# Kernel tuning notes

Hardware: AMD Instinct MI355X
Metric: run time of the kernel (lower is better)

The kernel has to match this reference:

```python
import jax, jax.numpy as jnp
import numpy as np

B, T = 16, 64
A = 6              # num_actions
E = 12288          # embed_size
DET = 4096         # deter_size
HID = 1024         # hidden_size
S, D = 32, 32      # stoch_size, discrete
UM = 0.01          # uniform_mix
CLIP = 1.0         # action_clip
EPS = 1e-3         # LayerNorm eps


def _ln(x, g, b):
    m = jnp.mean(x, -1, keepdims=True)
    v = jnp.var(x, -1, keepdims=True)
    return (x - m) * jax.lax.rsqrt(v + EPS) * g + b


def setup_inputs() -> dict:
    key = jax.random.key(0)
    ks = jax.random.split(key, 24)
    w = lambda k, i, o: (jax.random.normal(k, (i, o), jnp.float32) / np.sqrt(i))
    gum = lambda k, shp: -jnp.log(-jnp.log(jax.random.uniform(k, shp, jnp.float32, 1e-6, 1.0 - 1e-6)))
    is_firsts = (jax.random.uniform(ks[2], (B, T)) < 0.05).astype(jnp.float32)
    is_firsts = is_firsts.at[:, 0].set(1.0)
    return {
        'embed': jax.random.normal(ks[0], (B, T, E), jnp.float32),
        'prev_actions': jax.random.normal(ks[1], (B, T, A), jnp.float32),
        'is_firsts': is_firsts,
        'gumbel_prior': gum(ks[3], (B, T, S, D)),
        'gumbel_post': gum(ks[4], (B, T, S, D)),
        'w_init': jnp.zeros((DET,), jnp.float32),
        'W_img1': w(ks[5], S * D + A, HID), 'g_img1': jnp.ones((HID,)), 'b_img1': jnp.zeros((HID,)),
        'W_gru': w(ks[6], HID + DET, 3 * DET), 'g_gru': jnp.ones((3 * DET,)), 'b_gru': jnp.zeros((3 * DET,)),
        'W_img2a': w(ks[7], DET, HID), 'g_img2': jnp.ones((HID,)), 'b_img2': jnp.zeros((HID,)),
        'W_img2b': w(ks[8], HID, S * D), 'bb_img2': jnp.zeros((S * D,)),
        'W_obs': w(ks[9], E + DET, HID), 'g_obs': jnp.ones((HID,)), 'b_obs': jnp.zeros((HID,)),
        'W_obsb': w(ks[10], HID, S * D), 'bb_obs': jnp.zeros((S * D,)),
    }


def reference(embed, prev_actions, is_firsts, gumbel_prior, gumbel_post,
              w_init, W_img1, g_img1, b_img1, W_gru, g_gru, b_gru,
              W_img2a, g_img2, b_img2, W_img2b, bb_img2,
              W_obs, g_obs, b_obs, W_obsb, bb_obs):
    sg = jax.lax.stop_gradient

    def clip_act(a):
        return a * sg(CLIP / jnp.maximum(jnp.abs(a), CLIP))

    def prior_logits(deter):  # mlp_img2
        h = jax.nn.silu(_ln(deter @ W_img2a, g_img2, b_img2))
        return (h @ W_img2b + bb_img2).reshape(deter.shape[:-1] + (S, D))

    def mix_probs(logits):  # OneHotDist uniform mix
        p = jax.nn.softmax(logits, -1)
        return (1.0 - UM) * p + UM / D

    def st_sample(logits, g):  # straight-through gumbel-max sample
        p = mix_probs(logits)
        oh = jax.nn.one_hot(jnp.argmax(jnp.log(p) + g, -1), D, dtype=logits.dtype)
        return oh + p - sg(p)

    def st_mode(logits):
        p = mix_probs(logits)
        oh = jax.nn.one_hot(jnp.argmax(p, -1), D, dtype=logits.dtype)
        return oh + p - sg(p)

    # learned initial state (initial(): deter=tanh(w), stoch=mode, logits=0)
    init_deter = jnp.broadcast_to(jnp.tanh(w_init)[None], (B, DET))
    init_stoch = st_mode(prior_logits(init_deter))

    # observe() with prev_state=None zeroes the first action and starts from initial state
    prev_actions = prev_actions.at[:, 0].set(0.0)

    def step(carry, xs):
        stoch, deter, logits_post = carry
        a, e, f, gp, gq = xs
        a = clip_act(a)                                  # clip in forward()
        f1 = f[:, None]
        f3 = f[:, None, None]
        a = a * (1.0 - f1)
        stoch = stoch * (1.0 - f3) + init_stoch * f3
        deter = deter * (1.0 - f1) + init_deter * f1
        logits_post = logits_post * (1.0 - f3)           # initial logits are zeros
        a = clip_act(a)                                  # clipped again in forward_img()
        # mlp_img1
        x = jax.nn.silu(_ln(jnp.concatenate([stoch.reshape(B, S * D), a], -1) @ W_img1, g_img1, b_img1))
        # DreamerV2 GRU cell: single LN-linear -> reset/cand/update
        parts = _ln(jnp.concatenate([x, deter], -1) @ W_gru, g_gru, b_gru)
        reset, cand, update = jnp.split(parts, 3, -1)
        reset = jax.nn.sigmoid(reset)
        cand = jnp.tanh(reset * cand)
        update = jax.nn.sigmoid(update - 1.0)
        deter_new = update * cand + (1.0 - update) * deter
        # prior head
        lp = prior_logits(deter_new)
        stoch_prior = st_sample(lp, gp)
        # posterior head (mlp_obs1)
        h2 = jax.nn.silu(_ln(jnp.concatenate([e, deter_new], -1) @ W_obs, g_obs, b_obs))
        lq = (h2 @ W_obsb + bb_obs).reshape(B, S, D)
        stoch_post = st_sample(lq, gq)
        return (stoch_post, deter_new, lq), (stoch_post, deter_new, lq, stoch_prior, lp)

    carry0 = (init_stoch, init_deter, jnp.zeros((B, S, D), embed.dtype))
    xs = (jnp.swapaxes(prev_actions, 0, 1), jnp.swapaxes(embed, 0, 1), jnp.swapaxes(is_firsts, 0, 1),
          jnp.swapaxes(gumbel_prior, 0, 1), jnp.swapaxes(gumbel_post, 0, 1))
    _, outs = jax.lax.scan(step, carry0, xs)
    post_stoch, post_deter, post_logits, prior_stoch, prior_lg = [jnp.swapaxes(o, 0, 1) for o in outs]
    # pack posts and priors (prior deter == post deter) into one array [B,T,8192]
    return jnp.concatenate([post_stoch.reshape(B, T, S * D), post_deter,
                            post_logits.reshape(B, T, S * D),
                            prior_stoch.reshape(B, T, S * D),
                            prior_lg.reshape(B, T, S * D)], -1)
```

## Files before the change

### kernel.cpp

```cpp
#include <hip/hip_runtime.h>
#include <cmath>


#define B 16
#define T_STEPS 64
#define A_DIM 6
#define E_DIM 12288
#define DET 4096
#define HID 1024
#define SD 1024
#define OUT_C 8192
#define OUT_RSTRIDE (T_STEPS * OUT_C)

typedef float f2v __attribute__((ext_vector_type(2)));

__device__ __forceinline__ float block_sum(float v, float* red, int nw) {
#pragma unroll
  for (int m = 32; m >= 1; m >>= 1) v += __shfl_xor(v, m, 64);
  int wid = threadIdx.x >> 6;
  if ((threadIdx.x & 63) == 0) red[wid] = v;
  __syncthreads();
  if (wid == 0) {
    float s = ((int)threadIdx.x < nw) ? red[threadIdx.x] : 0.0f;
#pragma unroll
    for (int m = 8; m >= 1; m >>= 1) s += __shfl_xor(s, m, 16);
    if (threadIdx.x == 0) red[0] = s;
  }
  __syncthreads();
  float out = red[0];
  __syncthreads();
  return out;
}

__global__ __launch_bounds__(1024) void k_tanh(const float* __restrict__ w, float* __restrict__ o) {
  int i = blockIdx.x * 1024 + threadIdx.x;
  if (i < DET) o[i] = tanhf(w[i]);
}

__global__ __launch_bounds__(256) void k_prep(
    const float* __restrict__ isf, const float* __restrict__ pa, int t,
    const float* __restrict__ stoch_prev,
    const float* __restrict__ deter_prev, long deter_prev_stride,
    const float* __restrict__ init_stoch, const float* __restrict__ init_deter_row,
    float* __restrict__ stoch_in, float* __restrict__ deter_in, float* __restrict__ a_eff) {
  int r = blockIdx.x;
  float f = isf[r * T_STEPS + t];
  float omf = 1.0f - f;
  for (int c = threadIdx.x; c < SD; c += 256)
    stoch_in[r * SD + c] = stoch_prev[r * SD + c] * omf + init_stoch[r * SD + c] * f;
  for (int c = threadIdx.x; c < DET; c += 256)
    deter_in[r * DET + c] = deter_prev[(long)r * deter_prev_stride + c] * omf + init_deter_row[c] * f;
  if ((int)threadIdx.x < A_DIM) {
    float a = pa[(r * T_STEPS + t) * A_DIM + threadIdx.x];
    a = a * (1.0f / fmaxf(fabsf(a), 1.0f));
    a_eff[r * 8 + threadIdx.x] = a * omf;
  }
}

struct GemmArgs {
  const float* A0; long sA0; int cA0;
  const float* A1; long sA1;
  const float* W; int N; int Ktot; int KS; int nsplit;
  float* P;
};

template <bool NT>
__global__ __launch_bounds__(256) void k_gemm(GemmArgs g) {
  if ((int)blockIdx.y >= g.nsplit) return;
  const int tid = threadIdx.x;
  const int c0 = blockIdx.x * 512 + tid * 2;
  const int k0 = (int)blockIdx.y * g.KS;
  __shared__ float in_s[16][64];
  float acc[16][2];
#pragma unroll
  for (int r = 0; r < 16; r++) { acc[r][0] = 0.f; acc[r][1] = 0.f; }
  for (int kb = 0; kb < g.KS; kb += 64) {
    const int kbase = k0 + kb;
#pragma unroll
    for (int j = 0; j < 4; j++) {
      int ii = tid + j * 256;
      int r = ii >> 6, kk = ii & 63;
      int k = kbase + kk;
      float v = 0.f;
      if (k < g.cA0) v = g.A0[(long)r * g.sA0 + k];
      else if (k < g.Ktot) v = g.A1[(long)r * g.sA1 + (k - g.cA0)];
      in_s[r][kk] = v;
    }
    __syncthreads();
    if (kbase + 64 <= g.Ktot) {
      const float* wp = g.W + (size_t)kbase * g.N + c0;
#pragma unroll 4
      for (int kk = 0; kk < 64; kk++) {
        f2v w = NT ? __builtin_nontemporal_load((const f2v*)wp) : *(const f2v*)wp;
        wp += g.N;
#pragma unroll
        for (int r = 0; r < 16; r++) {
          acc[r][0] += in_s[r][kk] * w[0]; acc[r][1] += in_s[r][kk] * w[1];
        }
      }
    } else {
#pragma unroll 4
      for (int kk = 0; kk < 64; kk++) {
        int krow = kbase + kk; if (krow >= g.Ktot) krow = g.Ktot - 1;
        const f2v w = *(const f2v*)(g.W + (size_t)krow * g.N + c0);
#pragma unroll
        for (int r = 0; r < 16; r++) {
          acc[r][0] += in_s[r][kk] * w[0]; acc[r][1] += in_s[r][kk] * w[1];
        }
      }
    }
    __syncthreads();
  }
#pragma unroll
  for (int r = 0; r < 16; r++)
    *(f2v*)(g.P + ((size_t)blockIdx.y * 16 + r) * g.N + c0) = f2v{acc[r][0], acc[r][1]};
}

__global__ __launch_bounds__(1024) void k_fin(
    const float* __restrict__ P, int nP,
    const float* __restrict__ add, long ads,
    const float* __restrict__ gv, const float* __restrict__ bv,
    float* __restrict__ o) {
  int r = blockIdx.x, c = threadIdx.x;
  __shared__ float red[18];
  float v = add ? add[(size_t)r * ads + c] : 0.0f;
  for (int ks = 0; ks < nP; ks++) v += P[((size_t)ks * 16 + r) * HID + c];
  float m = block_sum(v, red, 16) * (1.0f / (float)HID);
  float d = v - m;
  float var = block_sum(d * d, red, 16) * (1.0f / (float)HID);
  float rs = 1.0f / sqrtf(var + 1e-3f);
  float y = d * rs * gv[c] + bv[c];
  float s = 1.0f / (1.0f + expf(-y));
  o[r * HID + c] = y * s;
}

__global__ __launch_bounds__(1024) void k_samp_init(
    const float* __restrict__ P, int nP, const float* __restrict__ bb,
    float* __restrict__ st) {
  int r = blockIdx.x, c = threadIdx.x;
  float acc = bb[c];
  for (int ks = 0; ks < nP; ks++) acc += P[((size_t)ks * 16 + r) * SD + c];
  int d = c & 31;
  float mx = acc;
#pragma unroll
  for (int m = 16; m >= 1; m >>= 1) mx = fmaxf(mx, __shfl_xor(mx, m, 32));
  float e = expf(acc - mx);
  float se = e;
#pragma unroll
  for (int m = 16; m >= 1; m >>= 1) se += __shfl_xor(se, m, 32);
  float p = 0.99f * (e / se) + 3.125e-4f;
  float by = p; int bi = d;
#pragma unroll
  for (int m = 16; m >= 1; m >>= 1) {
    float oy = __shfl_xor(by, m, 32);
    int oi = __shfl_xor(bi, m, 32);
    if (oy > by || (oy == by && oi < bi)) { by = oy; bi = oi; }
  }
  float oh = (d == bi) ? 1.0f : 0.0f;
  st[r * SD + c] = (oh + p) - p;
}

__global__ __launch_bounds__(256) void k_mm(const float* __restrict__ A, long lda,
                                            const float* __restrict__ Bw, int K,
                                            float* __restrict__ out, long ldo,
                                            const float* __restrict__ bias) {
  __shared__ float As[32][68];
  __shared__ float Bs[32][68];
  const int tid = threadIdx.x;
  const int tx = tid & 15, ty = tid >> 4;
  const int row0 = blockIdx.y * 64, col0 = blockIdx.x * 64;
  const int ar = tid >> 2, ak = (tid & 3) * 8;
  const int bk = tid >> 4, bc = (tid & 15) * 4;
  float acc[4][4] = {};
  const float* ap = A + (size_t)(row0 + ar) * lda + ak;
  const float* bp = Bw + (size_t)bk * HID + col0 + bc;
  for (int k0 = 0; k0 < K; k0 += 32) {
    float4 a0 = *(const float4*)(ap + k0);
    float4 a1 = *(const float4*)(ap + k0 + 4);
    float4 b0 = *(const float4*)(bp + (size_t)k0 * HID);
    float4 b1 = *(const float4*)(bp + (size_t)(k0 + 16) * HID);
    __syncthreads();
    As[ak + 0][ar] = a0.x; As[ak + 1][ar] = a0.y; As[ak + 2][ar] = a0.z; As[ak + 3][ar] = a0.w;
    As[ak + 4][ar] = a1.x; As[ak + 5][ar] = a1.y; As[ak + 6][ar] = a1.z; As[ak + 7][ar] = a1.w;
    *(float4*)&Bs[bk][bc] = b0;
    *(float4*)&Bs[bk + 16][bc] = b1;
    __syncthreads();
#pragma unroll
    for (int kk = 0; kk < 32; kk++) {
      float4 av = *(const float4*)&As[kk][ty * 4];
      float4 bv = *(const float4*)&Bs[kk][tx * 4];
      acc[0][0] += av.x * bv.x; acc[0][1] += av.x * bv.y; acc[0][2] += av.x * bv.z; acc[0][3] += av.x * bv.w;
      acc[1][0] += av.y * bv.x; acc[1][1] += av.y * bv.y; acc[1][2] += av.y * bv.z; acc[1][3] += av.y * bv.w;
      acc[2][0] += av.z * bv.x; acc[2][1] += av.z * bv.y; acc[2][2] += av.z * bv.z; acc[2][3] += av.z * bv.w;
      acc[3][0] += av.w * bv.x; acc[3][1] += av.w * bv.y; acc[3][2] += av.w * bv.z; acc[3][3] += av.w * bv.w;
    }
  }
#pragma unroll
  for (int i = 0; i < 4; i++) {
    float4 o;
    int col = col0 + tx * 4;
    o.x = acc[i][0] + (bias ? bias[col + 0] : 0.f);
    o.y = acc[i][1] + (bias ? bias[col + 1] : 0.f);
    o.z = acc[i][2] + (bias ? bias[col + 2] : 0.f);
    o.w = acc[i][3] + (bias ? bias[col + 3] : 0.f);
    *(float4*)(out + (size_t)(row0 + ty * 4 + i) * ldo + col) = o;
  }
}

__global__ __launch_bounds__(256) void k_ln_rows(float* __restrict__ h,
                                                 const float* __restrict__ gv,
                                                 const float* __restrict__ bv) {
  int row = blockIdx.x, c0 = threadIdx.x * 4;
  __shared__ float red[18];
  float4 v = *(const float4*)(h + (size_t)row * HID + c0);
  float lsum = (v.x + v.y) + (v.z + v.w);
  float m = block_sum(lsum, red, 4) * (1.0f / (float)HID);
  float dx = v.x - m, dy = v.y - m, dz = v.z - m, dw = v.w - m;
  float lv = (dx * dx + dy * dy) + (dz * dz + dw * dw);
  float var = block_sum(lv, red, 4) * (1.0f / (float)HID);
  float rs = 1.0f / sqrtf(var + 1e-3f);
  float4 o;
  float y0 = dx * rs * gv[c0] + bv[c0];         o.x = y0 / (1.0f + expf(-y0));
  float y1 = dy * rs * gv[c0 + 1] + bv[c0 + 1]; o.y = y1 / (1.0f + expf(-y1));
  float y2 = dz * rs * gv[c0 + 2] + bv[c0 + 2]; o.z = y2 / (1.0f + expf(-y2));
  float y3 = dw * rs * gv[c0 + 3] + bv[c0 + 3]; o.w = y3 / (1.0f + expf(-y3));
  *(float4*)(h + (size_t)row * HID + c0) = o;
}

__global__ __launch_bounds__(1024) void k_samp_prior(float* __restrict__ out,
                                                     const float* __restrict__ gum) {
  int m = blockIdx.x, c = threadIdx.x;
  float lp = out[(size_t)m * OUT_C + 7168 + c];
  int d = c & 31;
  float mx = lp;
#pragma unroll
  for (int mm = 16; mm >= 1; mm >>= 1) mx = fmaxf(mx, __shfl_xor(mx, mm, 32));
  float e = expf(lp - mx);
  float se = e;
#pragma unroll
  for (int mm = 16; mm >= 1; mm >>= 1) se += __shfl_xor(se, mm, 32);
  float p = 0.99f * (e / se) + 3.125e-4f;
  float y = logf(p) + gum[(size_t)m * SD + c];
  float by = y; int bi = d;
#pragma unroll
  for (int mm = 16; mm >= 1; mm >>= 1) {
    float oy = __shfl_xor(by, mm, 32);
    int oi = __shfl_xor(bi, mm, 32);
    if (oy > by || (oy == by && oi < bi)) { by = oy; bi = oi; }
  }
  float oh = (d == bi) ? 1.0f : 0.0f;
  out[(size_t)m * OUT_C + 6144 + c] = (oh + p) - p;
}

__global__ __launch_bounds__(256) void k_red(const float* __restrict__ P, int nP,
                                             float* __restrict__ S,
                                             float* __restrict__ red_s, float* __restrict__ red_q) {
  int chunk = blockIdx.x, r = blockIdx.y;
  int c = chunk * 1024 + threadIdx.x * 4;
  float4 s = {0, 0, 0, 0};
  for (int ks = 0; ks < nP; ks++) {
    float4 v = *(const float4*)(P + ((size_t)ks * 16 + r) * (3 * DET) + c);
    s.x += v.x; s.y += v.y; s.z += v.z; s.w += v.w;
  }
  *(float4*)(S + (size_t)r * (3 * DET) + c) = s;
  float sx = (s.x + s.y) + (s.z + s.w);
  float sq = (s.x * s.x + s.y * s.y) + (s.z * s.z + s.w * s.w);
  __shared__ float rbuf[8];
#pragma unroll
  for (int m = 32; m >= 1; m >>= 1) { sx += __shfl_xor(sx, m, 64); sq += __shfl_xor(sq, m, 64); }
  int wid = threadIdx.x >> 6;
  if ((threadIdx.x & 63) == 0) { rbuf[wid] = sx; rbuf[4 + wid] = sq; }
  __syncthreads();
  if (threadIdx.x == 0) {
    red_s[r * 12 + chunk] = (rbuf[0] + rbuf[1]) + (rbuf[2] + rbuf[3]);
    red_q[r * 12 + chunk] = (rbuf[4] + rbuf[5]) + (rbuf[6] + rbuf[7]);
  }
}

__global__ __launch_bounds__(1024) void k_gru_gate(
    const float* __restrict__ S, const float* __restrict__ red_s, const float* __restrict__ red_q,
    const float* __restrict__ g, const float* __restrict__ b,
    float* __restrict__ deter_in, float* __restrict__ deter_new,
    float* __restrict__ out_deter, const float* __restrict__ isf, int t,
    const float* __restrict__ init_deter) {
  int r = blockIdx.x;
  __shared__ float mv[2];
  if (threadIdx.x == 0) {
    float s = 0.f, q = 0.f;
    for (int k2 = 0; k2 < 12; k2++) { s += red_s[r * 12 + k2]; q += red_q[r * 12 + k2]; }
    float m = s * (1.0f / (float)(3 * DET));
    float var = q * (1.0f / (float)(3 * DET)) - m * m;
    mv[0] = m; mv[1] = 1.0f / sqrtf(var + 1e-3f);
  }
  __syncthreads();
  float m = mv[0], rs = mv[1];
  float ft = (t + 1 < T_STEPS) ? isf[r * T_STEPS + t + 1] : 0.0f;
  for (int j = threadIdx.x; j < DET; j += 1024) {
    float lr = (S[(size_t)r * (3 * DET) + j] - m) * rs * g[j] + b[j];
    float lc = (S[(size_t)r * (3 * DET) + j + DET] - m) * rs * g[j + DET] + b[j + DET];
    float lu = (S[(size_t)r * (3 * DET) + j + 2 * DET] - m) * rs * g[j + 2 * DET] + b[j + 2 * DET];
    float rr = 1.0f / (1.0f + expf(-lr));
    float cd = tanhf(rr * lc);
    float uu = 1.0f / (1.0f + expf(-(lu - 1.0f)));
    float dn = uu * cd + (1.0f - uu) * deter_in[r * DET + j];
    deter_new[r * DET + j] = dn;
    out_deter[(size_t)r * OUT_RSTRIDE + j] = dn;
    deter_in[r * DET + j] = dn * (1.0f - ft) + init_deter[j] * ft;
  }
}

__global__ __launch_bounds__(1024) void k_samp(
    const float* __restrict__ P, int nP, const float* __restrict__ bb,
    const float* __restrict__ gum, long gs,
    float* __restrict__ st, long ss, float* __restrict__ lg, long ls,
    const float* __restrict__ isf, const float* __restrict__ pa, int t,
    float* __restrict__ stoch_in, float* __restrict__ a_eff,
    const float* __restrict__ init_stoch) {
  int r = blockIdx.x, c = threadIdx.x;
  float acc = bb[c];
  for (int ks = 0; ks < nP; ks++) acc += P[((size_t)ks * 16 + r) * SD + c];
  int d = c & 31;
  float mx = acc;
#pragma unroll
  for (int m = 16; m >= 1; m >>= 1) mx = fmaxf(mx, __shfl_xor(mx, m, 32));
  float e = expf(acc - mx);
  float se = e;
#pragma unroll
  for (int m = 16; m >= 1; m >>= 1) se += __shfl_xor(se, m, 32);
  float p = 0.99f * (e / se) + 3.125e-4f;
  float y = logf(p) + gum[(long)r * gs + c];
  float by = y; int bi = d;
#pragma unroll
  for (int m = 16; m >= 1; m >>= 1) {
    float oy = __shfl_xor(by, m, 32);
    int oi = __shfl_xor(bi, m, 32);
    if (oy > by || (oy == by && oi < bi)) { by = oy; bi = oi; }
  }
  float oh = (d == bi) ? 1.0f : 0.0f;
  float outv = (oh + p) - p;
  st[(long)r * ss + c] = outv;
  lg[(long)r * ls + c] = acc;
  float fn = (t + 1 < T_STEPS) ? isf[r * T_STEPS + t + 1] : 0.0f;
  stoch_in[r * SD + c] = outv * (1.0f - fn) + init_stoch[r * SD + c] * fn;
  if (c < A_DIM) {
    float a = (t + 1 < T_STEPS) ? pa[(r * T_STEPS + t + 1) * A_DIM + c] : 0.0f;
    a = a * (1.0f / fmaxf(fabsf(a), 1.0f));
    a_eff[r * 8 + c] = a * (1.0f - fn);
  }
}

static inline GemmArgs mkargs(const float* A0, long sA0, int cA0,
                              const float* A1, long sA1,
                              const float* W, int N, int Ktot, int KS, int nsplit, float* P) {
  GemmArgs g; g.A0 = A0; g.sA0 = sA0; g.cA0 = cA0; g.A1 = A1; g.sA1 = sA1;
  g.W = W; g.N = N; g.Ktot = Ktot; g.KS = KS; g.nsplit = nsplit; g.P = P;
  return g;
}

extern "C" void kernel_launch(void* const* d_in, const int* in_sizes, int n_in,
                              void* d_out, int out_size, void* d_ws, size_t ws_size,
                              hipStream_t stream) {
  const float* embed  = (const float*)d_in[0];
  const float* pa     = (const float*)d_in[1];
  const float* isf    = (const float*)d_in[2];
  const float* gprior = (const float*)d_in[3];
  const float* gpost  = (const float*)d_in[4];
  const float* w_init = (const float*)d_in[5];
  const float* W1  = (const float*)d_in[6];
  const float* g1  = (const float*)d_in[7];
  const float* b1  = (const float*)d_in[8];
  const float* Wg  = (const float*)d_in[9];
  const float* gg  = (const float*)d_in[10];
  const float* bg  = (const float*)d_in[11];
  const float* W2a = (const float*)d_in[12];
  const float* g2  = (const float*)d_in[13];
  const float* b2  = (const float*)d_in[14];
  const float* W2b = (const float*)d_in[15];
  const float* bb2 = (const float*)d_in[16];
  const float* Wo  = (const float*)d_in[17];
  const float* go  = (const float*)d_in[18];
  const float* bo  = (const float*)d_in[19];
  const float* Wob = (const float*)d_in[20];
  const float* bbo = (const float*)d_in[21];
  float* out = (float*)d_out;
  float* ws  = (float*)d_ws;

  float* Pg    = ws;
  float* h_all = Pg;
  float* Sg    = Pg + 3932160;
  float* red_s = Sg + 196608;
  float* red_q = red_s + 192;
  float* Pimg1 = red_s + 512;
  float* Pb    = Pimg1 + 278528;
  float* Ps1   = Pb + 524288;
  float* st_   = Ps1 + 262144;
  float* init_stoch = st_;
  float* init_deter = st_ + 16384;
  float* stoch_in   = st_ + 20480;
  float* deter_in   = st_ + 36864;
  float* deter_new  = st_ + 102400;
  float* a_eff      = st_ + 167936;
  float* x          = st_ + 168064;
  float* h2         = st_ + 184448;

  k_mm<<<dim3(16, 16), 256, 0, stream>>>(embed, E_DIM, Wo, E_DIM, out + 5120, OUT_C, nullptr);

  k_tanh<<<4, 1024, 0, stream>>>(w_init, init_deter);
  k_gemm<true><<<dim3(2, 32), 256, 0, stream>>>(
      mkargs(init_deter, 0, DET, nullptr, 0, W2a, HID, DET, 128, 32, Pb));
  k_fin<<<16, 1024, 0, stream>>>(Pb, 32, nullptr, 0, g2, b2, x);
  k_gemm<true><<<dim3(2, 16), 256, 0, stream>>>(
      mkargs(x, HID, HID, nullptr, 0, W2b, SD, HID, 64, 16, Ps1));
  k_samp_init<<<16, 1024, 0, stream>>>(Ps1, 16, bb2, init_stoch);

  k_prep<<<16, 256, 0, stream>>>(isf, pa, 0, init_stoch, init_deter, 0,
                                 init_stoch, init_deter, stoch_in, deter_in, a_eff);

  for (int t = 0; t < T_STEPS; t++) {
    k_gemm<true><<<dim3(2, 17), 256, 0, stream>>>(
        mkargs(stoch_in, SD, SD, a_eff, 8, W1, HID, SD + A_DIM, 64, 17, Pimg1));
    k_fin<<<16, 1024, 0, stream>>>(Pimg1, 17, nullptr, 0, g1, b1, x);
    k_gemm<false><<<dim3(24, 20), 256, 0, stream>>>(
        mkargs(x, HID, HID, deter_in, DET, Wg, 3 * DET, HID + DET, 256, 20, Pg));
    k_red<<<dim3(12, 16), 256, 0, stream>>>(Pg, 20, Sg, red_s, red_q);
    k_gru_gate<<<16, 1024, 0, stream>>>(Sg, red_s, red_q, gg, bg, deter_in, deter_new,
                                        out + (size_t)t * OUT_C + 1024, isf, t, init_deter);
    k_gemm<true><<<dim3(2, 32), 256, 0, stream>>>(
        mkargs(deter_new, DET, DET, nullptr, 0, Wo + (size_t)E_DIM * HID, HID, DET, 128, 32, Pb));
    k_fin<<<16, 1024, 0, stream>>>(Pb, 32, out + (size_t)t * OUT_C + 5120, OUT_RSTRIDE,
                                   go, bo, h2);
    k_gemm<true><<<dim3(2, 16), 256, 0, stream>>>(
        mkargs(h2, HID, HID, nullptr, 0, Wob, SD, HID, 64, 16, Ps1));
    k_samp<<<16, 1024, 0, stream>>>(
        Ps1, 16, bbo, gpost + (size_t)t * SD, (long)T_STEPS * SD,
        out + (size_t)t * OUT_C + 0, OUT_RSTRIDE,
        out + (size_t)t * OUT_C + 5120, OUT_RSTRIDE,
        isf, pa, t, stoch_in, a_eff, init_stoch);
  }

  k_mm<<<dim3(16, 16), 256, 0, stream>>>(out + 1024, OUT_C, W2a, DET, h_all, HID, nullptr);
  k_ln_rows<<<1024, 256, 0, stream>>>(h_all, g2, b2);
  k_mm<<<dim3(16, 16), 256, 0, stream>>>(h_all, HID, W2b, HID, out + 7168, OUT_C, bb2);
  k_samp_prior<<<1024, 1024, 0, stream>>>(out, gprior);
}
```

Measured before the change: 11.30 ms.

## Fuse per-step GEMMs with their reductions via last-block atomic counters

Inside the time loop, the split-K GEMM launches and their follow-up reduce/LayerNorm/sampling kernels are merged into single kernels. In each one, the last block to finish (found with an atomic counter) sums the partials and applies the epilogue. The GRU gate is computed inside the obs-GEMM blocks, with deter_in ping-ponged between two buffers. This cuts per-step kernel launches from 9 to 5 and removes several launch gaps. The costs are that gate math is repeated across both column tiles, the final reduction runs on a single block, and correctness now depends on threadfence and atomic ordering.

```diff
diff --git a/kernel.cpp b/kernel.cpp
--- a/kernel.cpp
+++ b/kernel.cpp
@@ -13,6 +13,7 @@
 #define OUT_RSTRIDE (T_STEPS * OUT_C)
 
 typedef float f2v __attribute__((ext_vector_type(2)));
+typedef float f4v __attribute__((ext_vector_type(4)));
 
 __device__ __forceinline__ float block_sum(float v, float* red, int nw) {
 #pragma unroll
@@ -66,7 +67,6 @@
 
 template <bool NT>
 __global__ __launch_bounds__(256) void k_gemm(GemmArgs g) {
-  if ((int)blockIdx.y >= g.nsplit) return;
   const int tid = threadIdx.x;
   const int c0 = blockIdx.x * 512 + tid * 2;
   const int k0 = (int)blockIdx.y * g.KS;
@@ -118,12 +118,11 @@
 
 __global__ __launch_bounds__(1024) void k_fin(
     const float* __restrict__ P, int nP,
-    const float* __restrict__ add, long ads,
     const float* __restrict__ gv, const float* __restrict__ bv,
     float* __restrict__ o) {
   int r = blockIdx.x, c = threadIdx.x;
   __shared__ float red[18];
-  float v = add ? add[(size_t)r * ads + c] : 0.0f;
+  float v = 0.0f;
   for (int ks = 0; ks < nP; ks++) v += P[((size_t)ks * 16 + r) * HID + c];
   float m = block_sum(v, red, 16) * (1.0f / (float)HID);
   float d = v - m;
@@ -277,75 +276,267 @@
   }
 }
 
-__global__ __launch_bounds__(1024) void k_gru_gate(
-    const float* __restrict__ S, const float* __restrict__ red_s, const float* __restrict__ red_q,
-    const float* __restrict__ g, const float* __restrict__ b,
-    float* __restrict__ deter_in, float* __restrict__ deter_new,
-    float* __restrict__ out_deter, const float* __restrict__ isf, int t,
-    const float* __restrict__ init_deter) {
-  int r = blockIdx.x;
-  __shared__ float mv[2];
-  if (threadIdx.x == 0) {
+
+__global__ __launch_bounds__(256) void k_img1f(
+    const float* __restrict__ stoch_in, const float* __restrict__ a_eff,
+    const float* __restrict__ W, const float* __restrict__ gv, const float* __restrict__ bv,
+    float* __restrict__ P, float* __restrict__ xout, unsigned int* __restrict__ cnt) {
+  const int tid = threadIdx.x;
+  const int c0 = blockIdx.x * 512 + tid * 2;
+  const int kbase = (int)blockIdx.y * 64;
+  __shared__ float in_s[16][64];
+  __shared__ float red[18];
+  __shared__ unsigned int lastv;
+  float acc[16][2];
+#pragma unroll
+  for (int r = 0; r < 16; r++) { acc[r][0] = 0.f; acc[r][1] = 0.f; }
+#pragma unroll
+  for (int j = 0; j < 4; j++) {
+    int ii = tid + j * 256;
+    int r = ii >> 6, kk = ii & 63;
+    int k = kbase + kk;
+    float v = 0.f;
+    if (k < SD) v = stoch_in[r * SD + k];
+    else if (k < SD + A_DIM) v = a_eff[r * 8 + (k - SD)];
+    in_s[r][kk] = v;
+  }
+  __syncthreads();
+  if (kbase + 64 <= SD + A_DIM) {
+    const float* wp = W + (size_t)kbase * HID + c0;
+#pragma unroll 4
+    for (int kk = 0; kk < 64; kk++) {
+      f2v w = __builtin_nontemporal_load((const f2v*)wp);
+      wp += HID;
+#pragma unroll
+      for (int r = 0; r < 16; r++) {
+        acc[r][0] += in_s[r][kk] * w[0]; acc[r][1] += in_s[r][kk] * w[1];
+      }
+    }
+  } else {
+#pragma unroll 4
+    for (int kk = 0; kk < 64; kk++) {
+      int krow = kbase + kk; if (krow >= SD + A_DIM) krow = SD + A_DIM - 1;
+      const f2v w = *(const f2v*)(W + (size_t)krow * HID + c0);
+#pragma unroll
+      for (int r = 0; r < 16; r++) {
+        acc[r][0] += in_s[r][kk] * w[0]; acc[r][1] += in_s[r][kk] * w[1];
+      }
+    }
+  }
+#pragma unroll
+  for (int r = 0; r < 16; r++)
+    *(f2v*)(P + ((size_t)blockIdx.y * 16 + r) * HID + c0) = f2v{acc[r][0], acc[r][1]};
+  __threadfence();
+  __syncthreads();
+  if (tid == 0) lastv = atomicAdd(cnt, 1u);
+  __syncthreads();
+  if (lastv == 34u - 1u) {
+    if (tid == 0) atomicExch(cnt, 0u);
+    __threadfence();
+    const int c = tid * 4;
+    for (int r = 0; r < 16; r++) {
+      f4v v = {0, 0, 0, 0};
+      for (int ks = 0; ks < 17; ks++) {
+        f4v pv = *(const f4v*)(P + ((size_t)ks * 16 + r) * HID + c);
+        v[0] += pv[0]; v[1] += pv[1]; v[2] += pv[2]; v[3] += pv[3];
+      }
+      float lsum = (v[0] + v[1]) + (v[2] + v[3]);
+      float m = block_sum(lsum, red, 4) * (1.0f / (float)HID);
+      float d0 = v[0] - m, d1 = v[1] - m, d2 = v[2] - m, d3 = v[3] - m;
+      float lv = (d0 * d0 + d1 * d1) + (d2 * d2 + d3 * d3);
+      float var = block_sum(lv, red, 4) * (1.0f / (float)HID);
+      float rs = 1.0f / sqrtf(var + 1e-3f);
+      float dd[4] = {d0, d1, d2, d3};
+      f4v o;
+#pragma unroll
+      for (int j = 0; j < 4; j++) {
+        float y = dd[j] * rs * gv[c + j] + bv[c + j];
+        o[j] = y / (1.0f + expf(-y));
+      }
+      *(f4v*)(xout + (size_t)r * HID + c) = o;
+    }
+  }
+}
+
+__global__ __launch_bounds__(256) void k_obsf(
+    const float* __restrict__ Sg, const float* __restrict__ red_s, const float* __restrict__ red_q,
+    const float* __restrict__ gg, const float* __restrict__ bg,
+    const float* __restrict__ din_cur, float* __restrict__ din_next,
+    const float* __restrict__ init_deter, const float* __restrict__ isf, int t,
+    const float* __restrict__ W, const float* __restrict__ gv, const float* __restrict__ bv,
+    float* __restrict__ out, float* __restrict__ h2,
+    float* __restrict__ P, unsigned int* __restrict__ cnt) {
+  const int tid = threadIdx.x;
+  const int tile = blockIdx.x;
+  const int split = blockIdx.y;
+  const int c0 = tile * 512 + tid * 2;
+  const int j0 = split * 128;
+  __shared__ float dn_s[16][128];
+  __shared__ float mvf[16][3];
+  __shared__ float red[18];
+  __shared__ unsigned int lastv;
+  if (tid < 16) {
+    int r = tid;
     float s = 0.f, q = 0.f;
     for (int k2 = 0; k2 < 12; k2++) { s += red_s[r * 12 + k2]; q += red_q[r * 12 + k2]; }
     float m = s * (1.0f / (float)(3 * DET));
     float var = q * (1.0f / (float)(3 * DET)) - m * m;
-    mv[0] = m; mv[1] = 1.0f / sqrtf(var + 1e-3f);
-  }
-  __syncthreads();
-  float m = mv[0], rs = mv[1];
-  float ft = (t + 1 < T_STEPS) ? isf[r * T_STEPS + t + 1] : 0.0f;
-  for (int j = threadIdx.x; j < DET; j += 1024) {
-    float lr = (S[(size_t)r * (3 * DET) + j] - m) * rs * g[j] + b[j];
-    float lc = (S[(size_t)r * (3 * DET) + j + DET] - m) * rs * g[j + DET] + b[j + DET];
-    float lu = (S[(size_t)r * (3 * DET) + j + 2 * DET] - m) * rs * g[j + 2 * DET] + b[j + 2 * DET];
+    mvf[r][0] = m; mvf[r][1] = 1.0f / sqrtf(var + 1e-3f);
+    mvf[r][2] = (t + 1 < T_STEPS) ? isf[r * T_STEPS + t + 1] : 0.0f;
+  }
+  __syncthreads();
+  for (int e = tid; e < 16 * 128; e += 256) {
+    int r = e >> 7, jj = e & 127;
+    int j = j0 + jj;
+    float m = mvf[r][0], rs = mvf[r][1];
+    const float* Sr = Sg + (size_t)r * (3 * DET);
+    float lr = (Sr[j] - m) * rs * gg[j] + bg[j];
+    float lc = (Sr[j + DET] - m) * rs * gg[j + DET] + bg[j + DET];
+    float lu = (Sr[j + 2 * DET] - m) * rs * gg[j + 2 * DET] + bg[j + 2 * DET];
     float rr = 1.0f / (1.0f + expf(-lr));
     float cd = tanhf(rr * lc);
     float uu = 1.0f / (1.0f + expf(-(lu - 1.0f)));
-    float dn = uu * cd + (1.0f - uu) * deter_in[r * DET + j];
-    deter_new[r * DET + j] = dn;
-    out_deter[(size_t)r * OUT_RSTRIDE + j] = dn;
-    deter_in[r * DET + j] = dn * (1.0f - ft) + init_deter[j] * ft;
-  }
-}
-
-__global__ __launch_bounds__(1024) void k_samp(
-    const float* __restrict__ P, int nP, const float* __restrict__ bb,
-    const float* __restrict__ gum, long gs,
-    float* __restrict__ st, long ss, float* __restrict__ lg, long ls,
-    const float* __restrict__ isf, const float* __restrict__ pa, int t,
+    float dn = uu * cd + (1.0f - uu) * din_cur[r * DET + j];
+    dn_s[r][jj] = dn;
+    if (tile == 0) {
+      out[(size_t)(r * T_STEPS + t) * OUT_C + 1024 + j] = dn;
+      float ft = mvf[r][2];
+      din_next[r * DET + j] = dn * (1.0f - ft) + init_deter[j] * ft;
+    }
+  }
+  __syncthreads();
+  float acc[16][2];
+#pragma unroll
+  for (int r = 0; r < 16; r++) { acc[r][0] = 0.f; acc[r][1] = 0.f; }
+  for (int kb = 0; kb < 128; kb += 64) {
+    const float* wp = W + (size_t)(j0 + kb) * HID + c0;
+#pragma unroll 4
+    for (int kk = 0; kk < 64; kk++) {
+      f2v w = __builtin_nontemporal_load((const f2v*)wp);
+      wp += HID;
+#pragma unroll
+      for (int r = 0; r < 16; r++) {
+        float iv = dn_s[r][kb + kk];
+        acc[r][0] += iv * w[0]; acc[r][1] += iv * w[1];
+      }
+    }
+  }
+#pragma unroll
+  for (int r = 0; r < 16; r++)
+    *(f2v*)(P + ((size_t)split * 16 + r) * HID + c0) = f2v{acc[r][0], acc[r][1]};
+  __threadfence();
+  __syncthreads();
+  if (tid == 0) lastv = atomicAdd(cnt, 1u);
+  __syncthreads();
+  if (lastv == 64u - 1u) {
+    if (tid == 0) atomicExch(cnt, 0u);
+    __threadfence();
+    const int c = tid * 4;
+    for (int r = 0; r < 16; r++) {
+      f4v v = *(const f4v*)(out + (size_t)(r * T_STEPS + t) * OUT_C + 5120 + c);
+      for (int ks = 0; ks < 32; ks++) {
+        f4v pv = *(const f4v*)(P + ((size_t)ks * 16 + r) * HID + c);
+        v[0] += pv[0]; v[1] += pv[1]; v[2] += pv[2]; v[3] += pv[3];
+      }
+      float lsum = (v[0] + v[1]) + (v[2] + v[3]);
+      float m = block_sum(lsum, red, 4) * (1.0f / (float)HID);
+      float d0 = v[0] - m, d1 = v[1] - m, d2 = v[2] - m, d3 = v[3] - m;
+      float lv = (d0 * d0 + d1 * d1) + (d2 * d2 + d3 * d3);
+      float var = block_sum(lv, red, 4) * (1.0f / (float)HID);
+      float rs = 1.0f / sqrtf(var + 1e-3f);
+      float dd[4] = {d0, d1, d2, d3};
+      f4v o;
+#pragma unroll
+      for (int j = 0; j < 4; j++) {
+        float y = dd[j] * rs * gv[c + j] + bv[c + j];
+        o[j] = y / (1.0f + expf(-y));
+      }
+      *(f4v*)(h2 + (size_t)r * HID + c) = o;
+    }
+  }
+}
+
+__global__ __launch_bounds__(256) void k_postf(
+    const float* __restrict__ h2, const float* __restrict__ W,
+    const float* __restrict__ bb, const float* __restrict__ gum, long gs,
+    float* __restrict__ out, int t,
+    const float* __restrict__ isf, const float* __restrict__ pa,
     float* __restrict__ stoch_in, float* __restrict__ a_eff,
-    const float* __restrict__ init_stoch) {
-  int r = blockIdx.x, c = threadIdx.x;
-  float acc = bb[c];
-  for (int ks = 0; ks < nP; ks++) acc += P[((size_t)ks * 16 + r) * SD + c];
-  int d = c & 31;
-  float mx = acc;
-#pragma unroll
-  for (int m = 16; m >= 1; m >>= 1) mx = fmaxf(mx, __shfl_xor(mx, m, 32));
-  float e = expf(acc - mx);
-  float se = e;
-#pragma unroll
-  for (int m = 16; m >= 1; m >>= 1) se += __shfl_xor(se, m, 32);
-  float p = 0.99f * (e / se) + 3.125e-4f;
-  float y = logf(p) + gum[(long)r * gs + c];
-  float by = y; int bi = d;
-#pragma unroll
-  for (int m = 16; m >= 1; m >>= 1) {
-    float oy = __shfl_xor(by, m, 32);
-    int oi = __shfl_xor(bi, m, 32);
-    if (oy > by || (oy == by && oi < bi)) { by = oy; bi = oi; }
-  }
-  float oh = (d == bi) ? 1.0f : 0.0f;
-  float outv = (oh + p) - p;
-  st[(long)r * ss + c] = outv;
-  lg[(long)r * ls + c] = acc;
-  float fn = (t + 1 < T_STEPS) ? isf[r * T_STEPS + t + 1] : 0.0f;
-  stoch_in[r * SD + c] = outv * (1.0f - fn) + init_stoch[r * SD + c] * fn;
-  if (c < A_DIM) {
-    float a = (t + 1 < T_STEPS) ? pa[(r * T_STEPS + t + 1) * A_DIM + c] : 0.0f;
-    a = a * (1.0f / fmaxf(fabsf(a), 1.0f));
-    a_eff[r * 8 + c] = a * (1.0f - fn);
+    const float* __restrict__ init_stoch,
+    float* __restrict__ P, unsigned int* __restrict__ cnt) {
+  const int tid = threadIdx.x;
+  const int c0 = blockIdx.x * 512 + tid * 2;
+  const int kbase = (int)blockIdx.y * 64;
+  __shared__ float in_s[16][64];
+  __shared__ unsigned int lastv;
+  float acc[16][2];
+#pragma unroll
+  for (int r = 0; r < 16; r++) { acc[r][0] = 0.f; acc[r][1] = 0.f; }
+#pragma unroll
+  for (int j = 0; j < 4; j++) {
+    int ii = tid + j * 256;
+    int r = ii >> 6, kk = ii & 63;
+    in_s[r][kk] = h2[r * HID + kbase + kk];
+  }
+  __syncthreads();
+  {
+    const float* wp = W + (size_t)kbase * SD + c0;
+#pragma unroll 4
+    for (int kk = 0; kk < 64; kk++) {
+      f2v w = __builtin_nontemporal_load((const f2v*)wp);
+      wp += SD;
+#pragma unroll
+      for (int r = 0; r < 16; r++) {
+        acc[r][0] += in_s[r][kk] * w[0]; acc[r][1] += in_s[r][kk] * w[1];
+      }
+    }
+  }
+#pragma unroll
+  for (int r = 0; r < 16; r++)
+    *(f2v*)(P + ((size_t)blockIdx.y * 16 + r) * SD + c0) = f2v{acc[r][0], acc[r][1]};
+  __threadfence();
+  __syncthreads();
+  if (tid == 0) lastv = atomicAdd(cnt, 1u);
+  __syncthreads();
+  if (lastv == 32u - 1u) {
+    if (tid == 0) atomicExch(cnt, 0u);
+    __threadfence();
+    const int d = tid & 31;
+    for (int it = 0; it < 64; it++) {
+      int gi = it * 8 + (tid >> 5);
+      int r = gi >> 5, grp = gi & 31;
+      int c = grp * 32 + d;
+      float a = bb[c];
+      for (int ks = 0; ks < 16; ks++) a += P[((size_t)ks * 16 + r) * SD + c];
+      float mx = a;
+#pragma unroll
+      for (int m = 16; m >= 1; m >>= 1) mx = fmaxf(mx, __shfl_xor(mx, m, 32));
+      float e = expf(a - mx);
+      float se = e;
+#pragma unroll
+      for (int m = 16; m >= 1; m >>= 1) se += __shfl_xor(se, m, 32);
+      float p = 0.99f * (e / se) + 3.125e-4f;
+      float y = logf(p) + gum[(long)r * gs + c];
+      float by = y; int bi = d;
+#pragma unroll
+      for (int m = 16; m >= 1; m >>= 1) {
+        float oy = __shfl_xor(by, m, 32);
+        int oi = __shfl_xor(bi, m, 32);
+        if (oy > by || (oy == by && oi < bi)) { by = oy; bi = oi; }
+      }
+      float oh = (d == bi) ? 1.0f : 0.0f;
+      float outv = (oh + p) - p;
+      float* ob = out + (size_t)(r * T_STEPS + t) * OUT_C;
+      ob[c] = outv;
+      ob[5120 + c] = a;
+      float fn = (t + 1 < T_STEPS) ? isf[r * T_STEPS + t + 1] : 0.0f;
+      stoch_in[r * SD + c] = outv * (1.0f - fn) + init_stoch[r * SD + c] * fn;
+      if (c < A_DIM) {
+        float av = (t + 1 < T_STEPS) ? pa[(r * T_STEPS + t + 1) * A_DIM + c] : 0.0f;
+        av = av * (1.0f / fmaxf(fabsf(av), 1.0f));
+        a_eff[r * 8 + c] = av * (1.0f - fn);
+      }
+    }
   }
 }
 
@@ -390,6 +581,7 @@
   float* Sg    = Pg + 3932160;
   float* red_s = Sg + 196608;
   float* red_q = red_s + 192;
+  unsigned int* cnts = (unsigned int*)(red_s + 384);
   float* Pimg1 = red_s + 512;
   float* Pb    = Pimg1 + 278528;
   float* Ps1   = Pb + 524288;
@@ -397,45 +589,42 @@
   float* init_stoch = st_;
   float* init_deter = st_ + 16384;
   float* stoch_in   = st_ + 20480;
-  float* deter_in   = st_ + 36864;
-  float* deter_new  = st_ + 102400;
+  float* din0       = st_ + 36864;
+  float* din1       = st_ + 102400;
   float* a_eff      = st_ + 167936;
   float* x          = st_ + 168064;
   float* h2         = st_ + 184448;
 
+  hipMemsetAsync(cnts, 0, 64, stream);
+
   k_mm<<<dim3(16, 16), 256, 0, stream>>>(embed, E_DIM, Wo, E_DIM, out + 5120, OUT_C, nullptr);
 
   k_tanh<<<4, 1024, 0, stream>>>(w_init, init_deter);
   k_gemm<true><<<dim3(2, 32), 256, 0, stream>>>(
       mkargs(init_deter, 0, DET, nullptr, 0, W2a, HID, DET, 128, 32, Pb));
-  k_fin<<<16, 1024, 0, stream>>>(Pb, 32, nullptr, 0, g2, b2, x);
+  k_fin<<<16, 1024, 0, stream>>>(Pb, 32, g2, b2, x);
   k_gemm<true><<<dim3(2, 16), 256, 0, stream>>>(
       mkargs(x, HID, HID, nullptr, 0, W2b, SD, HID, 64, 16, Ps1));
   k_samp_init<<<16, 1024, 0, stream>>>(Ps1, 16, bb2, init_stoch);
 
   k_prep<<<16, 256, 0, stream>>>(isf, pa, 0, init_stoch, init_deter, 0,
-                                 init_stoch, init_deter, stoch_in, deter_in, a_eff);
-
+                                 init_stoch, init_deter, stoch_in, din0, a_eff);
+
+  const float* Wo2 = Wo + (size_t)E_DIM * HID;
   for (int t = 0; t < T_STEPS; t++) {
-    k_gemm<true><<<dim3(2, 17), 256, 0, stream>>>(
-        mkargs(stoch_in, SD, SD, a_eff, 8, W1, HID, SD + A_DIM, 64, 17, Pimg1));
-    k_fin<<<16, 1024, 0, stream>>>(Pimg1, 17, nullptr, 0, g1, b1, x);
+    float* din_cur  = (t & 1) ? din1 : din0;
+    float* din_next = (t & 1) ? din0 : din1;
+    k_img1f<<<dim3(2, 17), 256, 0, stream>>>(stoch_in, a_eff, W1, g1, b1, Pimg1, x, cnts + 0);
     k_gemm<false><<<dim3(24, 20), 256, 0, stream>>>(
-        mkargs(x, HID, HID, deter_in, DET, Wg, 3 * DET, HID + DET, 256, 20, Pg));
+        mkargs(x, HID, HID, din_cur, DET, Wg, 3 * DET, HID + DET, 256, 20, Pg));
     k_red<<<dim3(12, 16), 256, 0, stream>>>(Pg, 20, Sg, red_s, red_q);
-    k_gru_gate<<<16, 1024, 0, stream>>>(Sg, red_s, red_q, gg, bg, deter_in, deter_new,
-                                        out + (size_t)t * OUT_C + 1024, isf, t, init_deter);
-    k_gemm<true><<<dim3(2, 32), 256, 0, stream>>>(
-        mkargs(deter_new, DET, DET, nullptr, 0, Wo + (size_t)E_DIM * HID, HID, DET, 128, 32, Pb));
-    k_fin<<<16, 1024, 0, stream>>>(Pb, 32, out + (size_t)t * OUT_C + 5120, OUT_RSTRIDE,
-                                   go, bo, h2);
-    k_gemm<true><<<dim3(2, 16), 256, 0, stream>>>(
-        mkargs(h2, HID, HID, nullptr, 0, Wob, SD, HID, 64, 16, Ps1));
-    k_samp<<<16, 1024, 0, stream>>>(
-        Ps1, 16, bbo, gpost + (size_t)t * SD, (long)T_STEPS * SD,
-        out + (size_t)t * OUT_C + 0, OUT_RSTRIDE,
-        out + (size_t)t * OUT_C + 5120, OUT_RSTRIDE,
-        isf, pa, t, stoch_in, a_eff, init_stoch);
+    k_obsf<<<dim3(2, 32), 256, 0, stream>>>(Sg, red_s, red_q, gg, bg, din_cur, din_next,
+                                            init_deter, isf, t, Wo2, go, bo, out, h2,
+                                            Pb, cnts + 1);
+    k_postf<<<dim3(2, 16), 256, 0, stream>>>(h2, Wob, bbo,
+                                             gpost + (size_t)t * SD, (long)T_STEPS * SD,
+                                             out, t, isf, pa, stoch_in, a_eff, init_stoch,
+                                             Ps1, cnts + 2);
   }
 
   k_mm<<<dim3(16, 16), 256, 0, stream>>>(out + 1024, OUT_C, W2a, DET, h_all, HID, nullptr);
```

Result: slower. 23.59 ms (+108.8%).

## Fuse GRU gating into obs-projection GEMM and double the GRU split-K factor

Applied to the files above, without the earlier changes.

Merges the GRU gate kernel into the posterior-head deter×W_obs GEMM. Each block recomputes the gate for its 128-wide K slice into shared memory, and only tile 0 writes the outputs. deter_in/deter_new become ping-pong buffers to avoid read/write hazards. The GRU GEMM split-K rises from 20 to 40 when the workspace is large enough, to expose more parallelism, and the workspace is re-laid out as a shared arena. This removes one launch and a global round trip per step, at the cost of redundant gate computation across the two column tiles.

```diff
diff --git a/kernel.cpp b/kernel.cpp
--- a/kernel.cpp
+++ b/kernel.cpp
@@ -13,6 +13,7 @@
 #define OUT_RSTRIDE (T_STEPS * OUT_C)
 
 typedef float f2v __attribute__((ext_vector_type(2)));
+typedef float f4v __attribute__((ext_vector_type(4)));
 
 __device__ __forceinline__ float block_sum(float v, float* red, int nw) {
 #pragma unroll
@@ -277,36 +278,69 @@
   }
 }
 
-__global__ __launch_bounds__(1024) void k_gru_gate(
-    const float* __restrict__ S, const float* __restrict__ red_s, const float* __restrict__ red_q,
-    const float* __restrict__ g, const float* __restrict__ b,
-    float* __restrict__ deter_in, float* __restrict__ deter_new,
-    float* __restrict__ out_deter, const float* __restrict__ isf, int t,
-    const float* __restrict__ init_deter) {
-  int r = blockIdx.x;
-  __shared__ float mv[2];
-  if (threadIdx.x == 0) {
+__global__ __launch_bounds__(256) void k_obsg(
+    const float* __restrict__ Sg, const float* __restrict__ red_s, const float* __restrict__ red_q,
+    const float* __restrict__ gg, const float* __restrict__ bg,
+    const float* __restrict__ din_cur, float* __restrict__ din_next,
+    const float* __restrict__ init_deter, const float* __restrict__ isf, int t,
+    const float* __restrict__ W,
+    float* __restrict__ out, float* __restrict__ P) {
+  const int tid = threadIdx.x;
+  const int tile = blockIdx.x;
+  const int split = blockIdx.y;
+  const int c0 = tile * 512 + tid * 2;
+  const int j0 = split * 128;
+  __shared__ float dn_s[16][128];
+  __shared__ float mvf[16][3];
+  if (tid < 16) {
+    int r = tid;
     float s = 0.f, q = 0.f;
     for (int k2 = 0; k2 < 12; k2++) { s += red_s[r * 12 + k2]; q += red_q[r * 12 + k2]; }
     float m = s * (1.0f / (float)(3 * DET));
     float var = q * (1.0f / (float)(3 * DET)) - m * m;
-    mv[0] = m; mv[1] = 1.0f / sqrtf(var + 1e-3f);
-  }
-  __syncthreads();
-  float m = mv[0], rs = mv[1];
-  float ft = (t + 1 < T_STEPS) ? isf[r * T_STEPS + t + 1] : 0.0f;
-  for (int j = threadIdx.x; j < DET; j += 1024) {
-    float lr = (S[(size_t)r * (3 * DET) + j] - m) * rs * g[j] + b[j];
-    float lc = (S[(size_t)r * (3 * DET) + j + DET] - m) * rs * g[j + DET] + b[j + DET];
-    float lu = (S[(size_t)r * (3 * DET) + j + 2 * DET] - m) * rs * g[j + 2 * DET] + b[j + 2 * DET];
+    mvf[r][0] = m; mvf[r][1] = 1.0f / sqrtf(var + 1e-3f);
+    mvf[r][2] = (t + 1 < T_STEPS) ? isf[r * T_STEPS + t + 1] : 0.0f;
+  }
+  __syncthreads();
+  for (int e = tid; e < 16 * 128; e += 256) {
+    int r = e >> 7, jj = e & 127;
+    int j = j0 + jj;
+    float m = mvf[r][0], rs = mvf[r][1];
+    const float* Sr = Sg + (size_t)r * (3 * DET);
+    float lr = (Sr[j] - m) * rs * gg[j] + bg[j];
+    float lc = (Sr[j + DET] - m) * rs * gg[j + DET] + bg[j + DET];
+    float lu = (Sr[j + 2 * DET] - m) * rs * gg[j + 2 * DET] + bg[j + 2 * DET];
     float rr = 1.0f / (1.0f + expf(-lr));
     float cd = tanhf(rr * lc);
     float uu = 1.0f / (1.0f + expf(-(lu - 1.0f)));
-    float dn = uu * cd + (1.0f - uu) * deter_in[r * DET + j];
-    deter_new[r * DET + j] = dn;
-    out_deter[(size_t)r * OUT_RSTRIDE + j] = dn;
-    deter_in[r * DET + j] = dn * (1.0f - ft) + init_deter[j] * ft;
-  }
+    float dn = uu * cd + (1.0f - uu) * din_cur[r * DET + j];
+    dn_s[r][jj] = dn;
+    if (tile == 0) {
+      out[(size_t)(r * T_STEPS + t) * OUT_C + 1024 + j] = dn;
+      float ft = mvf[r][2];
+      din_next[r * DET + j] = dn * (1.0f - ft) + init_deter[j] * ft;
+    }
+  }
+  __syncthreads();
+  float acc[16][2];
+#pragma unroll
+  for (int r = 0; r < 16; r++) { acc[r][0] = 0.f; acc[r][1] = 0.f; }
+  for (int kb = 0; kb < 128; kb += 64) {
+    const float* wp = W + (size_t)(j0 + kb) * HID + c0;
+#pragma unroll 4
+    for (int kk = 0; kk < 64; kk++) {
+      f2v w = __builtin_nontemporal_load((const f2v*)wp);
+      wp += HID;
+#pragma unroll
+      for (int r = 0; r < 16; r++) {
+        float iv = dn_s[r][kb + kk];
+        acc[r][0] += iv * w[0]; acc[r][1] += iv * w[1];
+      }
+    }
+  }
+#pragma unroll
+  for (int r = 0; r < 16; r++)
+    *(f2v*)(P + ((size_t)split * 16 + r) * HID + c0) = f2v{acc[r][0], acc[r][1]};
 }
 
 __global__ __launch_bounds__(1024) void k_samp(
@@ -385,20 +419,26 @@
   float* out = (float*)d_out;
   float* ws  = (float*)d_ws;
 
-  float* Pg    = ws;
-  float* h_all = Pg;
-  float* Sg    = Pg + 3932160;
+  const size_t STATE_FLOATS = 196608 + 512 + 200832;
+  int NSPLIT = 40, KSG = 128;
+  if (ws_size < ((size_t)40 * 16 * 12288 + STATE_FLOATS) * 4) { NSPLIT = 20; KSG = 256; }
+  const size_t ASZ = (size_t)NSPLIT * 16 * 12288;
+
+  float* arena = ws;
+  float* Pg    = arena;
+  float* h_all = arena;
+  float* Pimg1 = arena;
+  float* Pb    = arena + ASZ - 786432;
+  float* Ps1   = arena + ASZ - 262144;
+  float* Sg    = arena + ASZ;
   float* red_s = Sg + 196608;
   float* red_q = red_s + 192;
-  float* Pimg1 = red_s + 512;
-  float* Pb    = Pimg1 + 278528;
-  float* Ps1   = Pb + 524288;
-  float* st_   = Ps1 + 262144;
+  float* st_   = red_s + 512;
   float* init_stoch = st_;
   float* init_deter = st_ + 16384;
   float* stoch_in   = st_ + 20480;
-  float* deter_in   = st_ + 36864;
-  float* deter_new  = st_ + 102400;
+  float* din0       = st_ + 36864;
+  float* din1       = st_ + 102400;
   float* a_eff      = st_ + 167936;
   float* x          = st_ + 168064;
   float* h2         = st_ + 184448;
@@ -414,19 +454,20 @@
   k_samp_init<<<16, 1024, 0, stream>>>(Ps1, 16, bb2, init_stoch);
 
   k_prep<<<16, 256, 0, stream>>>(isf, pa, 0, init_stoch, init_deter, 0,
-                                 init_stoch, init_deter, stoch_in, deter_in, a_eff);
-
+                                 init_stoch, init_deter, stoch_in, din0, a_eff);
+
+  const float* Wo2 = Wo + (size_t)E_DIM * HID;
   for (int t = 0; t < T_STEPS; t++) {
+    float* din_cur  = (t & 1) ? din1 : din0;
+    float* din_next = (t & 1) ? din0 : din1;
     k_gemm<true><<<dim3(2, 17), 256, 0, stream>>>(
         mkargs(stoch_in, SD, SD, a_eff, 8, W1, HID, SD + A_DIM, 64, 17, Pimg1));
     k_fin<<<16, 1024, 0, stream>>>(Pimg1, 17, nullptr, 0, g1, b1, x);
-    k_gemm<false><<<dim3(24, 20), 256, 0, stream>>>(
-        mkargs(x, HID, HID, deter_in, DET, Wg, 3 * DET, HID + DET, 256, 20, Pg));
-    k_red<<<dim3(12, 16), 256, 0, stream>>>(Pg, 20, Sg, red_s, red_q);
-    k_gru_gate<<<16, 1024, 0, stream>>>(Sg, red_s, red_q, gg, bg, deter_in, deter_new,
-                                        out + (size_t)t * OUT_C + 1024, isf, t, init_deter);
-    k_gemm<true><<<dim3(2, 32), 256, 0, stream>>>(
-        mkargs(deter_new, DET, DET, nullptr, 0, Wo + (size_t)E_DIM * HID, HID, DET, 128, 32, Pb));
+    k_gemm<false><<<dim3(24, NSPLIT), 256, 0, stream>>>(
+        mkargs(x, HID, HID, din_cur, DET, Wg, 3 * DET, HID + DET, KSG, NSPLIT, Pg));
+    k_red<<<dim3(12, 16), 256, 0, stream>>>(Pg, NSPLIT, Sg, red_s, red_q);
+    k_obsg<<<dim3(2, 32), 256, 0, stream>>>(Sg, red_s, red_q, gg, bg, din_cur, din_next,
+                                            init_deter, isf, t, Wo2, out, Pb);
     k_fin<<<16, 1024, 0, stream>>>(Pb, 32, out + (size_t)t * OUT_C + 5120, OUT_RSTRIDE,
                                    go, bo, h2);
     k_gemm<true><<<dim3(2, 16), 256, 0, stream>>>(
```

Result: slower. 12.04 ms (+6.6%).
